# Kernel tuning notes

Hardware: AMD Instinct MI355X
Metric: run time of the kernel (lower is better)

Reference implementation:

```python
import math
import jax, jax.numpy as jnp
import numpy as np

SCALE = 1.0
OFFSET = 0.0
B, D, R = 524288, 64, 256


def setup_inputs() -> dict:
    key = jax.random.key(0)
    k1, k2, k3 = jax.random.split(key, 3)
    y = jax.random.uniform(k1, (B, 1), dtype=jnp.float32)  # in [0,1)
    x = jax.random.normal(k2, (B, D), dtype=jnp.float32)
    W = jax.random.normal(k3, (D, R), dtype=jnp.float32) * 0.05
    b = jnp.zeros((R,), dtype=jnp.float32)
    logdet = jnp.zeros((B,), dtype=jnp.float32)
    base_points = jnp.linspace(0.0, 1.0, R, dtype=jnp.float32)
    return {"y": y, "x": x, "W": W, "b": b, "logdet": logdet, "base_points": base_points}


def reference(y, x, W, b, logdet, base_points):
    # f(x): linear layer -> [B, R] logits; softmax + cumsum gives monotone CDF-like features
    basefeatures = jnp.cumsum(jax.nn.softmax(x @ W + b, axis=1), axis=1)  # [B, R]
    # bucketize: number of boundaries <= y, minus 1  == searchsorted(side='right') - 1
    start = jnp.searchsorted(base_points, y[:, 0], side="right") - 1  # [B] in [0, R-2]
    i = jnp.arange(basefeatures.shape[0])
    x0 = base_points[start][:, None]            # [B,1]
    x1 = base_points[start + 1][:, None]        # [B,1]
    f0 = basefeatures[i, start][:, None]        # [B,1]
    f1 = basefeatures[i, start + 1][:, None]    # [B,1]
    slope = (f1 - f0) / (x1 - x0)               # [B,1]
    z = SCALE * (f0 + slope * (y - x0)) + OFFSET
    dlogdet = math.log(SCALE) + jnp.log(jnp.abs(slope[:, 0]))
    return z, x, logdet + dlogdet
```

## Files before the change

kernel.cpp:

```cpp
#include <hip/hip_runtime.h>
#include <hip/hip_bf16.h>


#define NB 524288
#define NWT (NB / 16)

typedef __attribute__((ext_vector_type(4))) float f32x4;
typedef __attribute__((ext_vector_type(4))) unsigned int u32x4;
typedef __attribute__((ext_vector_type(8))) __bf16 bf16x8;

#define LOG2E 1.4426950408889634f

static __device__ __forceinline__ unsigned short f2b(float f) {
    unsigned u = __builtin_bit_cast(unsigned, f);
    u += 0x7fffu + ((u >> 16) & 1u);
    return (unsigned short)(u >> 16);
}
static __device__ __forceinline__ unsigned pk2t(float a, float b) {
    return (__builtin_bit_cast(unsigned, a) >> 16) | (__builtin_bit_cast(unsigned, b) & 0xffff0000u);
}

__global__ __launch_bounds__(512, 4) void interp1d_kernel(
    const float* __restrict__ y, const float* __restrict__ x,
    const float* __restrict__ W, const float* __restrict__ bias,
    const float* __restrict__ logdet, const float* __restrict__ bp,
    float* __restrict__ out)
{
    __shared__ unsigned short sW[2 * 16 * 64 * 8];
    __shared__ float sBP[256];
    __shared__ float sBias[256];

    const int t = threadIdx.x;

    if (t < 256) {
        sBP[t]   = bp[t];
        sBias[t] = bias[t] * LOG2E;
    }
    {
        const int col = t & 255;
        const int k0  = (t >> 8) << 5;
        const int lane16lo = col & 15;
        const int n = col >> 4;
        for (int kk = 0; kk < 32; ++kk) {
            int k = k0 + kk;
            float wv = W[k * 256 + col] * LOG2E;
            int lane16 = ((k >> 3) & 3) * 16 + lane16lo;
            int kb = k >> 5, i = k & 7;
            sW[((kb * 16 + n) * 64 + lane16) * 8 + i] = f2b(wv);
        }
    }
    __syncthreads();

    const int lane = t & 63;
    const int colb = lane & 15;
    const int kH   = lane >> 4;
    const int nw   = gridDim.x << 3;

    int wt = (blockIdx.x << 3) | (t >> 6);

    f32x4 v0 = {}, v1 = {}, v2 = {}, v3 = {};
    float yv = 0.f, ldv = 0.f;
    if (wt < NWT) {
        const float* xr = x + (size_t)((wt << 4) + colb) * 64 + (kH << 3);
        v0 = *reinterpret_cast<const f32x4*>(xr);
        v1 = *reinterpret_cast<const f32x4*>(xr + 4);
        v2 = *reinterpret_cast<const f32x4*>(xr + 32);
        v3 = *reinterpret_cast<const f32x4*>(xr + 36);
        yv  = y[(wt << 4) + colb];
        ldv = logdet[(wt << 4) + colb];
    }

    for (; wt < NWT; wt += nw) {
        const int m0 = wt << 4;
        const int wtn = wt + nw;

        f32x4 n0 = {}, n1 = {}, n2 = {}, n3 = {};
        float yn = 0.f, ldn = 0.f;
        if (wtn < NWT) {
            const float* xr = x + (size_t)((wtn << 4) + colb) * 64 + (kH << 3);
            n0 = *reinterpret_cast<const f32x4*>(xr);
            n1 = *reinterpret_cast<const f32x4*>(xr + 4);
            n2 = *reinterpret_cast<const f32x4*>(xr + 32);
            n3 = *reinterpret_cast<const f32x4*>(xr + 36);
            yn  = y[(wtn << 4) + colb];
            ldn = logdet[(wtn << 4) + colb];
        }

        asm volatile("" ::: "memory");

        float* xo = out + NB + (size_t)(m0 + colb) * 64 + (kH << 3);
        __builtin_nontemporal_store(v0, reinterpret_cast<f32x4*>(xo));
        __builtin_nontemporal_store(v1, reinterpret_cast<f32x4*>(xo + 4));
        __builtin_nontemporal_store(v2, reinterpret_cast<f32x4*>(xo + 32));
        __builtin_nontemporal_store(v3, reinterpret_cast<f32x4*>(xo + 36));

        u32x4 pa, pb;
        pa[0] = pk2t(v0[0], v0[1]); pa[1] = pk2t(v0[2], v0[3]);
        pa[2] = pk2t(v1[0], v1[1]); pa[3] = pk2t(v1[2], v1[3]);
        pb[0] = pk2t(v2[0], v2[1]); pb[1] = pk2t(v2[2], v2[3]);
        pb[2] = pk2t(v3[0], v3[1]); pb[3] = pk2t(v3[2], v3[3]);
        bf16x8 a0 = __builtin_bit_cast(bf16x8, pa);
        bf16x8 a1 = __builtin_bit_cast(bf16x8, pb);

        int s = (int)floorf(yv * 255.0f);
        s = min(254, max(0, s));
        s += (sBP[s + 1] <= yv) ? 1 : 0;
        s = min(s, 254);
        s -= (sBP[s] > yv) ? 1 : 0;
        s = max(s, 0);

        const int sb  = s >> 4,  so  = s & 15;
        const int sb1 = (s + 1) >> 4, so1 = (s + 1) & 15;
        float m[4], pm[4];
        #pragma unroll
        for (int j = 0; j < 4; ++j) {
            m[j]  = ((kH << 2) + j <= so)  ? 1.f : 0.f;
            pm[j] = ((kH << 2) + j == so1) ? 1.f : 0.f;
        }

        float denom = 0.f, f0s = 0.f, p1 = 0.f;
        #pragma unroll
        for (int n = 0; n < 16; ++n) {
            bf16x8 w0 = *reinterpret_cast<const bf16x8*>(&sW[(n * 64 + lane) * 8]);
            bf16x8 w1 = *reinterpret_cast<const bf16x8*>(&sW[((16 + n) * 64 + lane) * 8]);
            f32x4 c = *reinterpret_cast<const f32x4*>(&sBias[(n << 4) + (kH << 2)]);
            c = __builtin_amdgcn_mfma_f32_16x16x32_bf16(w0, a0, c, 0, 0, 0);
            c = __builtin_amdgcn_mfma_f32_16x16x32_bf16(w1, a1, c, 0, 0, 0);
            float e0 = __builtin_amdgcn_exp2f(c[0]);
            float e1 = __builtin_amdgcn_exp2f(c[1]);
            float e2 = __builtin_amdgcn_exp2f(c[2]);
            float e3 = __builtin_amdgcn_exp2f(c[3]);
            float bs = (e0 + e1) + (e2 + e3);
            denom += bs;
            float t0 = fmaf(e3, m[3], fmaf(e2, m[2], fmaf(e1, m[1], e0 * m[0])));
            float tp = fmaf(e3, pm[3], fmaf(e2, pm[2], fmaf(e1, pm[1], e0 * pm[0])));
            f0s += (n < sb) ? bs : ((n == sb) ? t0 : 0.f);
            p1  += (n == sb1) ? tp : 0.f;
        }

        denom += __shfl_xor(denom, 16, 64);
        f0s   += __shfl_xor(f0s,   16, 64);
        p1    += __shfl_xor(p1,    16, 64);
        denom += __shfl_xor(denom, 32, 64);
        f0s   += __shfl_xor(f0s,   32, 64);
        p1    += __shfl_xor(p1,    32, 64);

        if (kH == 0) {
            float x0 = sBP[s], x1 = sBP[s + 1];
            float inv = 1.0f / denom;
            float f0 = f0s * inv;
            float slope = (p1 * inv) / (x1 - x0);
            __builtin_nontemporal_store(fmaf(slope, yv - x0, f0), out + m0 + colb);
            __builtin_nontemporal_store(ldv + __logf(fabsf(slope)),
                                        out + (size_t)NB * 65 + m0 + colb);
        }

        if (wtn < NWT) {
            v0 = n0; v1 = n1; v2 = n2; v3 = n3;
            yv = yn; ldv = ldn;
        }
    }
}

extern "C" void kernel_launch(void* const* d_in, const int* in_sizes, int n_in,
                              void* d_out, int out_size, void* d_ws, size_t ws_size,
                              hipStream_t stream) {
    (void)in_sizes; (void)n_in; (void)out_size; (void)d_ws; (void)ws_size;
    const float* y      = (const float*)d_in[0];
    const float* x      = (const float*)d_in[1];
    const float* W      = (const float*)d_in[2];
    const float* b      = (const float*)d_in[3];
    const float* logdet = (const float*)d_in[4];
    const float* bp     = (const float*)d_in[5];
    float* out = (float*)d_out;
    interp1d_kernel<<<dim3(1024), dim3(512), 0, stream>>>(y, x, W, b, logdet, bp, out);
}
```

Before: 59.59 us.

## Coalesce x loads/stores and reshuffle bf16 A-fragments through per-wave LDS

Each wave now loads and stores its 16x64 tile of x as contiguous float4 chunks indexed by lane, instead of strided per-row pieces, so global accesses are fully coalesced. The bf16-packed values are written to a padded per-wave LDS buffer and read back in the MFMA A-fragment layout. The occupancy hint in launch bounds drops from 4 to 2 blocks per CU. This adds an LDS round trip per tile, and correctness relies on intra-wave ordering since no barrier is used.

```diff
diff --git a/kernel.cpp b/kernel.cpp
--- a/kernel.cpp
+++ b/kernel.cpp
@@ -6,7 +6,6 @@
 #define NWT (NB / 16)
 
 typedef __attribute__((ext_vector_type(4))) float f32x4;
-typedef __attribute__((ext_vector_type(4))) unsigned int u32x4;
 typedef __attribute__((ext_vector_type(8))) __bf16 bf16x8;
 
 #define LOG2E 1.4426950408889634f
@@ -20,13 +19,14 @@
     return (__builtin_bit_cast(unsigned, a) >> 16) | (__builtin_bit_cast(unsigned, b) & 0xffff0000u);
 }
 
-__global__ __launch_bounds__(512, 4) void interp1d_kernel(
+__global__ __launch_bounds__(512, 2) void interp1d_kernel(
     const float* __restrict__ y, const float* __restrict__ x,
     const float* __restrict__ W, const float* __restrict__ bias,
     const float* __restrict__ logdet, const float* __restrict__ bp,
     float* __restrict__ out)
 {
     __shared__ unsigned short sW[2 * 16 * 64 * 8];
+    __shared__ unsigned short sX[8 * 16 * 72];
     __shared__ float sBP[256];
     __shared__ float sBias[256];
 
@@ -54,6 +54,7 @@
     const int lane = t & 63;
     const int colb = lane & 15;
     const int kH   = lane >> 4;
+    unsigned short* myX = &sX[(t >> 6) * (16 * 72)];
     const int nw   = gridDim.x << 3;
 
     int wt = (blockIdx.x << 3) | (t >> 6);
@@ -61,11 +62,8 @@
     f32x4 v0 = {}, v1 = {}, v2 = {}, v3 = {};
     float yv = 0.f, ldv = 0.f;
     if (wt < NWT) {
-        const float* xr = x + (size_t)((wt << 4) + colb) * 64 + (kH << 3);
-        v0 = *reinterpret_cast<const f32x4*>(xr);
-        v1 = *reinterpret_cast<const f32x4*>(xr + 4);
-        v2 = *reinterpret_cast<const f32x4*>(xr + 32);
-        v3 = *reinterpret_cast<const f32x4*>(xr + 36);
+        const f32x4* xg = reinterpret_cast<const f32x4*>(x) + (size_t)wt * 256;
+        v0 = xg[lane]; v1 = xg[64 + lane]; v2 = xg[128 + lane]; v3 = xg[192 + lane];
         yv  = y[(wt << 4) + colb];
         ldv = logdet[(wt << 4) + colb];
     }
@@ -77,30 +75,38 @@
         f32x4 n0 = {}, n1 = {}, n2 = {}, n3 = {};
         float yn = 0.f, ldn = 0.f;
         if (wtn < NWT) {
-            const float* xr = x + (size_t)((wtn << 4) + colb) * 64 + (kH << 3);
-            n0 = *reinterpret_cast<const f32x4*>(xr);
-            n1 = *reinterpret_cast<const f32x4*>(xr + 4);
-            n2 = *reinterpret_cast<const f32x4*>(xr + 32);
-            n3 = *reinterpret_cast<const f32x4*>(xr + 36);
+            const f32x4* xg = reinterpret_cast<const f32x4*>(x) + (size_t)wtn * 256;
+            n0 = xg[lane]; n1 = xg[64 + lane]; n2 = xg[128 + lane]; n3 = xg[192 + lane];
             yn  = y[(wtn << 4) + colb];
             ldn = logdet[(wtn << 4) + colb];
         }
 
         asm volatile("" ::: "memory");
 
-        float* xo = out + NB + (size_t)(m0 + colb) * 64 + (kH << 3);
-        __builtin_nontemporal_store(v0, reinterpret_cast<f32x4*>(xo));
-        __builtin_nontemporal_store(v1, reinterpret_cast<f32x4*>(xo + 4));
-        __builtin_nontemporal_store(v2, reinterpret_cast<f32x4*>(xo + 32));
-        __builtin_nontemporal_store(v3, reinterpret_cast<f32x4*>(xo + 36));
+        f32x4* xo = reinterpret_cast<f32x4*>(out + NB) + (size_t)wt * 256;
+        __builtin_nontemporal_store(v0, xo + lane);
+        __builtin_nontemporal_store(v1, xo + 64 + lane);
+        __builtin_nontemporal_store(v2, xo + 128 + lane);
+        __builtin_nontemporal_store(v3, xo + 192 + lane);
 
-        u32x4 pa, pb;
-        pa[0] = pk2t(v0[0], v0[1]); pa[1] = pk2t(v0[2], v0[3]);
-        pa[2] = pk2t(v1[0], v1[1]); pa[3] = pk2t(v1[2], v1[3]);
-        pb[0] = pk2t(v2[0], v2[1]); pb[1] = pk2t(v2[2], v2[3]);
-        pb[2] = pk2t(v3[0], v3[1]); pb[3] = pk2t(v3[2], v3[3]);
-        bf16x8 a0 = __builtin_bit_cast(bf16x8, pa);
-        bf16x8 a1 = __builtin_bit_cast(bf16x8, pb);
+        {
+            uint2 w; int c, row, pos;
+            c = lane;        row = c >> 4; pos = c & 15;
+            w.x = pk2t(v0[0], v0[1]); w.y = pk2t(v0[2], v0[3]);
+            *reinterpret_cast<uint2*>(&myX[row * 72 + pos * 4]) = w;
+            c = 64 + lane;   row = c >> 4; pos = c & 15;
+            w.x = pk2t(v1[0], v1[1]); w.y = pk2t(v1[2], v1[3]);
+            *reinterpret_cast<uint2*>(&myX[row * 72 + pos * 4]) = w;
+            c = 128 + lane;  row = c >> 4; pos = c & 15;
+            w.x = pk2t(v2[0], v2[1]); w.y = pk2t(v2[2], v2[3]);
+            *reinterpret_cast<uint2*>(&myX[row * 72 + pos * 4]) = w;
+            c = 192 + lane;  row = c >> 4; pos = c & 15;
+            w.x = pk2t(v3[0], v3[1]); w.y = pk2t(v3[2], v3[3]);
+            *reinterpret_cast<uint2*>(&myX[row * 72 + pos * 4]) = w;
+        }
+
+        bf16x8 a0 = *reinterpret_cast<const bf16x8*>(&myX[colb * 72 + (kH << 3)]);
+        bf16x8 a1 = *reinterpret_cast<const bf16x8*>(&myX[colb * 72 + 32 + (kH << 3)]);
 
         int s = (int)floorf(yv * 255.0f);
         s = min(254, max(0, s));
```

Result: faster. 56.04 us (-6.0%).
